# Kernel optimization log

Hardware: AMD Instinct MI355X
Metric: run time of the kernel (lower is better)

## Reference

```python
import jax, jax.numpy as jnp
import numpy as np

B, IN, HID, OUT, E, NMAP = 16384, 64, 128, 1, 64, 1000


def setup_inputs() -> dict:
    key = jax.random.key(0)
    ks = jax.random.split(key, 7)
    x = jax.random.normal(ks[0], (B, IN), dtype=jnp.float32)
    num = jax.random.randint(ks[1], (B,), 0, NMAP, dtype=jnp.int64)
    c = jax.random.randint(ks[2], (NMAP,), 0, E, dtype=jnp.int64)
    # per-expert 2-layer MLP params (kaiming-ish scale)
    W1 = jax.random.normal(ks[3], (E, IN, HID), dtype=jnp.float32) * (1.0 / np.sqrt(IN))
    b1 = jnp.zeros((E, HID), dtype=jnp.float32)
    W2 = jax.random.normal(ks[4], (E, HID, OUT), dtype=jnp.float32) * (1.0 / np.sqrt(HID))
    b2 = jnp.zeros((E, OUT), dtype=jnp.float32)
    return {"x": x, "num": num, "c": c, "W1": W1, "b1": b1, "W2": W2, "b2": b2}


def reference(x, num, c, W1, b1, W2, b2):
    # per-sample expert id: c[num[i]]
    e = c[num]                                   # [B]
    # gather each sample's expert weights and run batched MLP
    h = jnp.einsum('bi,bih->bh', x, W1[e]) + b1[e]   # [B, HID]
    h = jax.nn.relu(h)
    y = jnp.einsum('bh,bho->bo', h, W2[e]) + b2[e]   # [B, OUT]
    return jax.nn.sigmoid(y)
```

## Files before the change

kernel.cpp:

```cpp
#include <hip/hip_runtime.h>
#include <math.h>


#define B_N    16384
#define IN_D   64
#define HID_D  128
#define E_N    64
#define NGRP   16
#define GRP_S  (B_N / NGRP)
#define CAPC   256

typedef __attribute__((ext_vector_type(8))) short v8s;
typedef __attribute__((ext_vector_type(4))) float v4f;

__device__ __forceinline__ short f2bf(float f) {
    unsigned int u = __float_as_uint(f);
    u += 0x7fffu + ((u >> 16) & 1u);
    return (short)(u >> 16);
}

__global__ __launch_bounds__(256) void moe_fused(
    const float* __restrict__ x, const int* __restrict__ num,
    const int* __restrict__ c, const float* __restrict__ W1,
    const float* __restrict__ b1, const float* __restrict__ W2,
    const float* __restrict__ b2, float* __restrict__ out)
{
    __shared__ v8s   s_frag[IN_D * HID_D / 8];
    __shared__ int   s_list[CAPC];
    __shared__ float s_yw[4][CAPC];
    __shared__ int   s_cnt;

    const int tid = threadIdx.x;
    const int e   = blockIdx.x & (E_N - 1);
    const int g   = blockIdx.x >> 6;

    const int  s0 = g * GRP_S + tid * 4;
    const int4 nv = *(const int4*)&num[s0];

    const int f0    = tid * 4;
    const int w     = f0 >> 8, nt = (f0 >> 7) & 1, kh = (f0 >> 6) & 1;
    const int fq    = (f0 >> 4) & 3;
    const int hbase = 32 * w + 16 * nt + (f0 & 15);
    const float* W1e = W1 + (size_t)e * (IN_D * HID_D);
    float4 wv[8];
    #pragma unroll
    for (int j = 0; j < 8; ++j)
        wv[j] = *(const float4*)&W1e[(32 * kh + 8 * fq + j) * HID_D + hbase];

    if (tid == 0) s_cnt = 0;
    __syncthreads();

    const int e0 = c[nv.x], e1 = c[nv.y], e2 = c[nv.z], e3 = c[nv.w];
    if (e0 == e) { int p = atomicAdd(&s_cnt, 1); if (p < CAPC) s_list[p] = s0;     }
    if (e1 == e) { int p = atomicAdd(&s_cnt, 1); if (p < CAPC) s_list[p] = s0 + 1; }
    if (e2 == e) { int p = atomicAdd(&s_cnt, 1); if (p < CAPC) s_list[p] = s0 + 2; }
    if (e3 == e) { int p = atomicAdd(&s_cnt, 1); if (p < CAPC) s_list[p] = s0 + 3; }

    v8s t[4];
    #pragma unroll
    for (int j = 0; j < 8; ++j) {
        t[0][j] = f2bf(wv[j].x); t[1][j] = f2bf(wv[j].y);
        t[2][j] = f2bf(wv[j].z); t[3][j] = f2bf(wv[j].w);
    }
    #pragma unroll
    for (int i = 0; i < 4; ++i) s_frag[f0 + i] = t[i];

    const int wave = __builtin_amdgcn_readfirstlane(tid >> 6);
    const int lane = tid & 63, l16 = lane & 15, qd = lane >> 4;
    const int h0   = 32 * wave + l16, h1 = h0 + 16;
    const float b1v0 = b1[e * HID_D + h0], b1v1 = b1[e * HID_D + h1];
    const float w2v0 = W2[e * HID_D + h0], w2v1 = W2[e * HID_D + h1];
    const float b2v  = b2[e];
    __syncthreads();

    v8s bfrag[2][2];
    #pragma unroll
    for (int n2 = 0; n2 < 2; ++n2)
        #pragma unroll
        for (int k2 = 0; k2 < 2; ++k2)
            bfrag[n2][k2] = s_frag[((wave * 2 + n2) * 2 + k2) * 64 + lane];

    const int total  = min(s_cnt, CAPC);
    const int ntiles = (total + 15) >> 4;
    for (int mt = 0; mt < ntiles; ++mt) {
        const int idx = mt * 16 + l16;
        const int s   = s_list[min(idx, total - 1)];
        const float4* row = (const float4*)(x + (size_t)s * IN_D);

        const float4 r0 = row[2 * qd],     r1 = row[2 * qd + 1];
        const float4 r2 = row[8 + 2 * qd], r3 = row[8 + 2 * qd + 1];
        v8s a0, a1;
        a0[0]=f2bf(r0.x); a0[1]=f2bf(r0.y); a0[2]=f2bf(r0.z); a0[3]=f2bf(r0.w);
        a0[4]=f2bf(r1.x); a0[5]=f2bf(r1.y); a0[6]=f2bf(r1.z); a0[7]=f2bf(r1.w);
        a1[0]=f2bf(r2.x); a1[1]=f2bf(r2.y); a1[2]=f2bf(r2.z); a1[3]=f2bf(r2.w);
        a1[4]=f2bf(r3.x); a1[5]=f2bf(r3.y); a1[6]=f2bf(r3.z); a1[7]=f2bf(r3.w);

        v4f acc0 = {0.f, 0.f, 0.f, 0.f};
        v4f acc1 = {0.f, 0.f, 0.f, 0.f};
        acc0 = __builtin_amdgcn_mfma_f32_16x16x32_bf16(a0, bfrag[0][0], acc0, 0, 0, 0);
        acc0 = __builtin_amdgcn_mfma_f32_16x16x32_bf16(a1, bfrag[0][1], acc0, 0, 0, 0);
        acc1 = __builtin_amdgcn_mfma_f32_16x16x32_bf16(a0, bfrag[1][0], acc1, 0, 0, 0);
        acc1 = __builtin_amdgcn_mfma_f32_16x16x32_bf16(a1, bfrag[1][1], acc1, 0, 0, 0);

        #pragma unroll
        for (int r = 0; r < 4; ++r) {
            float v = fmaxf(acc0[r] + b1v0, 0.f) * w2v0
                    + fmaxf(acc1[r] + b1v1, 0.f) * w2v1;
            v += __shfl_xor(v, 1);
            v += __shfl_xor(v, 2);
            v += __shfl_xor(v, 4);
            v += __shfl_xor(v, 8);
            if (l16 == 0) s_yw[wave][mt * 16 + qd * 4 + r] = v;
        }
    }
    __syncthreads();

    for (int i = tid; i < total; i += 256) {
        const float tv = s_yw[0][i] + s_yw[1][i] + s_yw[2][i] + s_yw[3][i] + b2v;
        out[s_list[i]] = 1.0f / (1.0f + expf(-tv));
    }
}

extern "C" void kernel_launch(void* const* d_in, const int* in_sizes, int n_in,
                              void* d_out, int out_size, void* d_ws, size_t ws_size,
                              hipStream_t stream)
{
    const float* x   = (const float*)d_in[0];
    const int*   num = (const int*)  d_in[1];
    const int*   c   = (const int*)  d_in[2];
    const float* W1  = (const float*)d_in[3];
    const float* b1  = (const float*)d_in[4];
    const float* W2  = (const float*)d_in[5];
    const float* b2  = (const float*)d_in[6];
    float*       out = (float*)d_out;
    (void)d_ws; (void)ws_size;

    moe_fused<<<dim3(E_N * NGRP), dim3(256), 0, stream>>>(x, num, c, W1, b1, W2, b2, out);
}
```

Baseline: 73.94 us.

## Load MFMA B-fragments directly from global and aggregate list atomics per wave

Each lane now loads its own W1 elements for the MFMA B fragments straight from global memory and converts them in registers, which removes the shared-memory staging buffer and one block barrier. Sample-list insertion uses wave ballots and popcounts with a single atomicAdd per wave instead of one per matching sample. The trade is scalar, less coalesced global loads (32 per lane) in place of float4 loads, and lower LDS use that may allow more blocks per CU.

After: 74.26 us. Within noise of the previous version (+0.4%).

```diff
diff --git a/kernel.cpp b/kernel.cpp
--- a/kernel.cpp
+++ b/kernel.cpp
@@ -25,60 +25,69 @@
     const float* __restrict__ b1, const float* __restrict__ W2,
     const float* __restrict__ b2, float* __restrict__ out)
 {
-    __shared__ v8s   s_frag[IN_D * HID_D / 8];
     __shared__ int   s_list[CAPC];
     __shared__ float s_yw[4][CAPC];
     __shared__ int   s_cnt;
 
-    const int tid = threadIdx.x;
-    const int e   = blockIdx.x & (E_N - 1);
-    const int g   = blockIdx.x >> 6;
+    const int tid  = threadIdx.x;
+    const int e    = blockIdx.x & (E_N - 1);
+    const int g    = blockIdx.x >> 6;
+    const int lane = tid & 63;
+    const int wave = __builtin_amdgcn_readfirstlane(tid >> 6);
+    const int l16  = lane & 15, qd = lane >> 4;
 
     const int  s0 = g * GRP_S + tid * 4;
     const int4 nv = *(const int4*)&num[s0];
 
-    const int f0    = tid * 4;
-    const int w     = f0 >> 8, nt = (f0 >> 7) & 1, kh = (f0 >> 6) & 1;
-    const int fq    = (f0 >> 4) & 3;
-    const int hbase = 32 * w + 16 * nt + (f0 & 15);
-    const float* W1e = W1 + (size_t)e * (IN_D * HID_D);
-    float4 wv[8];
+    const float* W1e  = W1 + (size_t)e * (IN_D * HID_D);
+    const float* wbase = W1e + 8 * qd * HID_D + 32 * wave + l16;
+    float bw[2][2][8];
     #pragma unroll
-    for (int j = 0; j < 8; ++j)
-        wv[j] = *(const float4*)&W1e[(32 * kh + 8 * fq + j) * HID_D + hbase];
+    for (int kh = 0; kh < 2; ++kh)
+        #pragma unroll
+        for (int j = 0; j < 8; ++j) {
+            const float* r = wbase + (32 * kh + j) * HID_D;
+            bw[0][kh][j] = r[0];
+            bw[1][kh][j] = r[16];
+        }
+
+    const int h0  = 32 * wave + l16, h1 = h0 + 16;
+    const float b1v0 = b1[e * HID_D + h0], b1v1 = b1[e * HID_D + h1];
+    const float w2v0 = W2[e * HID_D + h0], w2v1 = W2[e * HID_D + h1];
+    const float b2v  = b2[e];
 
     if (tid == 0) s_cnt = 0;
     __syncthreads();
 
+    const unsigned long long lmask = (1ull << lane) - 1ull;
     const int e0 = c[nv.x], e1 = c[nv.y], e2 = c[nv.z], e3 = c[nv.w];
-    if (e0 == e) { int p = atomicAdd(&s_cnt, 1); if (p < CAPC) s_list[p] = s0;     }
-    if (e1 == e) { int p = atomicAdd(&s_cnt, 1); if (p < CAPC) s_list[p] = s0 + 1; }
-    if (e2 == e) { int p = atomicAdd(&s_cnt, 1); if (p < CAPC) s_list[p] = s0 + 2; }
-    if (e3 == e) { int p = atomicAdd(&s_cnt, 1); if (p < CAPC) s_list[p] = s0 + 3; }
-
-    v8s t[4];
-    #pragma unroll
-    for (int j = 0; j < 8; ++j) {
-        t[0][j] = f2bf(wv[j].x); t[1][j] = f2bf(wv[j].y);
-        t[2][j] = f2bf(wv[j].z); t[3][j] = f2bf(wv[j].w);
-    }
-    #pragma unroll
-    for (int i = 0; i < 4; ++i) s_frag[f0 + i] = t[i];
-
-    const int wave = __builtin_amdgcn_readfirstlane(tid >> 6);
-    const int lane = tid & 63, l16 = lane & 15, qd = lane >> 4;
-    const int h0   = 32 * wave + l16, h1 = h0 + 16;
-    const float b1v0 = b1[e * HID_D + h0], b1v1 = b1[e * HID_D + h1];
-    const float w2v0 = W2[e * HID_D + h0], w2v1 = W2[e * HID_D + h1];
-    const float b2v  = b2[e];
-    __syncthreads();
+    const bool h0b = (e0 == e), h1b = (e1 == e), h2b = (e2 == e), h3b = (e3 == e);
+    const unsigned long long m0 = __ballot(h0b), m1 = __ballot(h1b);
+    const unsigned long long m2 = __ballot(h2b), m3 = __ballot(h3b);
+    const int c0 = __popcll(m0), c1 = __popcll(m1), c2 = __popcll(m2);
+    const int ctot = c0 + c1 + c2 + __popcll(m3);
+    int base = 0;
+    if (lane == 0 && ctot) base = atomicAdd(&s_cnt, ctot);
+    base = __shfl(base, 0);
+    if (h0b) { const int p = base + __popcll(m0 & lmask);
+               if (p < CAPC) s_list[p] = s0;     }
+    if (h1b) { const int p = base + c0 + __popcll(m1 & lmask);
+               if (p < CAPC) s_list[p] = s0 + 1; }
+    if (h2b) { const int p = base + c0 + c1 + __popcll(m2 & lmask);
+               if (p < CAPC) s_list[p] = s0 + 2; }
+    if (h3b) { const int p = base + c0 + c1 + c2 + __popcll(m3 & lmask);
+               if (p < CAPC) s_list[p] = s0 + 3; }
 
     v8s bfrag[2][2];
     #pragma unroll
-    for (int n2 = 0; n2 < 2; ++n2)
+    for (int nt = 0; nt < 2; ++nt)
         #pragma unroll
-        for (int k2 = 0; k2 < 2; ++k2)
-            bfrag[n2][k2] = s_frag[((wave * 2 + n2) * 2 + k2) * 64 + lane];
+        for (int kh = 0; kh < 2; ++kh)
+            #pragma unroll
+            for (int j = 0; j < 8; ++j)
+                bfrag[nt][kh][j] = f2bf(bw[nt][kh][j]);
+
+    __syncthreads();
 
     const int total  = min(s_cnt, CAPC);
     const int ntiles = (total + 15) >> 4;
```
